# Optimization experiments

Hardware: AMD Instinct MI355X
Metric: run time of the kernel (lower is better)

The kernel has to match this reference:

```python
import jax, jax.numpy as jnp
import numpy as np

D = 1024
NUM_HEADS = 16
HEAD_DIM = D // NUM_HEADS
INIT_VALUES = 1e-4


def setup_inputs() -> dict:
    key = jax.random.key(0)
    ks = jax.random.split(key, 24)
    s = 0.02
    inp = {
        "v": jax.random.normal(ks[0], (8, 2048, D), dtype=jnp.float32),
        "l": jax.random.normal(ks[1], (8, 512, D), dtype=jnp.float32),
        "ln_v_g": jnp.ones((D,), jnp.float32),
        "ln_v_b": jnp.zeros((D,), jnp.float32),
        "ln_l_g": jnp.ones((D,), jnp.float32),
        "ln_l_b": jnp.zeros((D,), jnp.float32),
        "gamma_v": jnp.full((D,), INIT_VALUES, jnp.float32),
        "gamma_l": jnp.full((D,), INIT_VALUES, jnp.float32),
    }
    names = ["Wq_v2l", "Wk_v2l", "Wv_v2l", "Wo_v2l", "Wq_l2v", "Wk_l2v", "Wv_l2v", "Wo_l2v"]
    for i, n in enumerate(names):
        inp[n] = jax.random.normal(ks[2 + i], (D, D), dtype=jnp.float32) * s
        inp[n.replace("W", "b")] = jnp.zeros((D,), jnp.float32)
    return inp


def layer_norm(x, g, b, eps=1e-5):
    mu = jnp.mean(x, axis=-1, keepdims=True)
    var = jnp.var(x, axis=-1, keepdims=True)
    return (x - mu) * jax.lax.rsqrt(var + eps) * g + b


def mha(q_in, k_in, v_in, Wq, bq, Wk, bk, Wv, bv, Wo, bo):
    B, Sq, _ = q_in.shape
    Sk = k_in.shape[1]
    # torch Linear: x @ W.T + b
    q = (q_in @ Wq.T + bq).reshape(B, Sq, NUM_HEADS, HEAD_DIM)
    k = (k_in @ Wk.T + bk).reshape(B, Sk, NUM_HEADS, HEAD_DIM)
    v = (v_in @ Wv.T + bv).reshape(B, Sk, NUM_HEADS, HEAD_DIM)
    scores = jnp.einsum("bqhd,bkhd->bhqk", q, k) / np.sqrt(HEAD_DIM).astype(np.float32)
    attn = jax.nn.softmax(scores, axis=-1)
    ctx = jnp.einsum("bhqk,bkhd->bqhd", attn, v).reshape(B, Sq, D)
    return ctx @ Wo.T + bo


def reference(v, l, ln_v_g, ln_v_b, ln_l_g, ln_l_b, gamma_v, gamma_l,
              Wq_v2l, bq_v2l, Wk_v2l, bk_v2l, Wv_v2l, bv_v2l, Wo_v2l, bo_v2l,
              Wq_l2v, bq_l2v, Wk_l2v, bk_l2v, Wv_l2v, bv_l2v, Wo_l2v, bo_l2v):
    # eval mode: dropout and drop_path are identity
    v_norm = layer_norm(v, ln_v_g, ln_v_b)
    l_norm = layer_norm(l, ln_l_g, ln_l_b)
    updated_v = mha(v_norm, l_norm, l_norm,
                    Wq_v2l, bq_v2l, Wk_v2l, bk_v2l, Wv_v2l, bv_v2l, Wo_v2l, bo_v2l)
    updated_l = mha(l_norm, v_norm, v_norm,
                    Wq_l2v, bq_l2v, Wk_l2v, bk_l2v, Wv_l2v, bv_l2v, Wo_l2v, bo_l2v)
    v_out = v + gamma_v * updated_v
    l_out = l + gamma_l * updated_l
    return (v_out, l_out)
```

## Files before the change

kernel.cpp:

```cpp
#include <hip/hip_runtime.h>
#include <hip/hip_bf16.h>
#include <stdint.h>

typedef __bf16 bf16x8 __attribute__((ext_vector_type(8)));
typedef float f32x4 __attribute__((ext_vector_type(4)));
typedef float f32x16 __attribute__((ext_vector_type(16)));
typedef uint32_t u32x4 __attribute__((ext_vector_type(4)));
typedef unsigned short u16;

typedef __attribute__((address_space(1))) void as1_void;
typedef __attribute__((address_space(3))) void as3_void;

#define BAR() __builtin_amdgcn_s_barrier()
#define VMCNT(n) asm volatile("s_waitcnt vmcnt(" #n ")" ::: "memory")
#define LGKM0() asm volatile("s_waitcnt lgkmcnt(0)" ::: "memory")

__device__ __forceinline__ u16 f2bf(float f) {
  uint32_t u = __float_as_uint(f);
  u += 0x7fffu + ((u >> 16) & 1u);
  return (u16)(u >> 16);
}

struct Seg {
  const u16* W;
  const float* bias;
  u16* outb;
  float* outf;
  const float* res;
  const float* gamma;
  int mode;
  int sk;
  float ascale;
};

__global__ __launch_bounds__(256) void cvt8_kernel(
    const float4* s0, const float4* s1, const float4* s2, const float4* s3,
    const float4* s4, const float4* s5, const float4* s6, const float4* s7,
    ushort4* d0, ushort4* d1, ushort4* d2, ushort4* d3,
    ushort4* d4, ushort4* d5, ushort4* d6, ushort4* d7) {
  const float4* s; ushort4* d;
  switch (blockIdx.y) {
    case 0: s = s0; d = d0; break;
    case 1: s = s1; d = d1; break;
    case 2: s = s2; d = d2; break;
    case 3: s = s3; d = d3; break;
    case 4: s = s4; d = d4; break;
    case 5: s = s5; d = d5; break;
    case 6: s = s6; d = d6; break;
    default: s = s7; d = d7; break;
  }
  int i = blockIdx.x * 256 + threadIdx.x;
  float4 v = s[i];
  ushort4 o;
  o.x = f2bf(v.x); o.y = f2bf(v.y); o.z = f2bf(v.z); o.w = f2bf(v.w);
  d[i] = o;
}

__global__ __launch_bounds__(256) void ln_kernel(const float* __restrict__ x,
                                                 const float* __restrict__ g,
                                                 const float* __restrict__ b,
                                                 u16* __restrict__ out) {
  int row = blockIdx.x;
  int t = threadIdx.x;
  const float4* xr = (const float4*)(x + (size_t)row * 1024);
  float4 v = xr[t];
  float s = v.x + v.y + v.z + v.w;
  float s2 = v.x * v.x + v.y * v.y + v.z * v.z + v.w * v.w;
#pragma unroll
  for (int off = 1; off < 64; off <<= 1) {
    s += __shfl_xor(s, off);
    s2 += __shfl_xor(s2, off);
  }
  __shared__ float red[8];
  int wv = t >> 6;
  if ((t & 63) == 0) { red[wv] = s; red[4 + wv] = s2; }
  __syncthreads();
  s = red[0] + red[1] + red[2] + red[3];
  s2 = red[4] + red[5] + red[6] + red[7];
  float mu = s * (1.0f / 1024.0f);
  float var = s2 * (1.0f / 1024.0f) - mu * mu;
  float rstd = rsqrtf(var + 1e-5f);
  const float4 gv = ((const float4*)g)[t];
  const float4 bv = ((const float4*)b)[t];
  ushort4 o;
  o.x = f2bf((v.x - mu) * rstd * gv.x + bv.x);
  o.y = f2bf((v.y - mu) * rstd * gv.y + bv.y);
  o.z = f2bf((v.z - mu) * rstd * gv.z + bv.z);
  o.w = f2bf((v.w - mu) * rstd * gv.w + bv.w);
  ((ushort4*)out)[(size_t)row * 256 + t] = o;
}

__global__ __launch_bounds__(256, 3) void gemm_v7(
    const u16* __restrict__ A, Seg s0, Seg s1, Seg s2,
    int mtiles, int ntiles) {
  const int K = 1024;
  int hwid = blockIdx.x;
  int xcd = hwid & 7, q = hwid >> 3;
  int mchunk = mtiles >> 3;
  int mt = xcd * mchunk + q / ntiles;
  int nt = q % ntiles;
  int m0 = mt * 128;
  int si = nt >> 3;
  Seg seg = (si == 0) ? s0 : (si == 1) ? s1 : s2;
  int nl0 = (nt & 7) * 128;

  int t = threadIdx.x, lane = t & 63, wv = t >> 6;
  int wr = wv >> 1, wc = wv & 1;
  int lr = lane & 15, lg = lane >> 4;

  __shared__ u16 SA[3][128 * 32];
  __shared__ u16 SB[3][128 * 32];

  int row0 = t >> 2, c0 = t & 3;
  int sco = (c0 ^ ((row0 >> 1) & 3)) * 8;
  const u16* gA0 = A + (size_t)(m0 + row0) * K + sco;
  const u16* gB0 = seg.W + (size_t)(nl0 + row0) * K + sco;

  auto STAGE = [&](int slot, int kt) {
    __builtin_amdgcn_global_load_lds((const as1_void*)(gA0 + kt * 32),
                                     (as3_void*)(&SA[slot][0] + t * 8), 16, 0, 0);
    __builtin_amdgcn_global_load_lds((const as1_void*)(gA0 + (size_t)64 * K + kt * 32),
                                     (as3_void*)(&SA[slot][0] + 2048 + t * 8), 16, 0, 0);
    __builtin_amdgcn_global_load_lds((const as1_void*)(gB0 + kt * 32),
                                     (as3_void*)(&SB[slot][0] + t * 8), 16, 0, 0);
    __builtin_amdgcn_global_load_lds((const as1_void*)(gB0 + (size_t)64 * K + kt * 32),
                                     (as3_void*)(&SB[slot][0] + 2048 + t * 8), 16, 0, 0);
  };

  f32x4 acc[4][4] = {};

  STAGE(0, 0); STAGE(1, 1); STAGE(2, 2);
  VMCNT(8);
  BAR();

  int slot = 0;
  const int NKT = K / 32;
#pragma unroll 1
  for (int kt = 0; kt < NKT; ++kt) {
    bf16x8 aX[4], bX[4];
#pragma unroll
    for (int m = 0; m < 4; ++m) {
      int row = wr * 64 + m * 16 + lr;
      aX[m] = *(const bf16x8*)(&SA[slot][0] + row * 32 + ((lg ^ ((row >> 1) & 3)) * 8));
    }
#pragma unroll
    for (int n = 0; n < 4; ++n) {
      int row = wc * 64 + n * 16 + lr;
      bX[n] = *(const bf16x8*)(&SB[slot][0] + row * 32 + ((lg ^ ((row >> 1) & 3)) * 8));
    }
    LGKM0();
    BAR();
    if (kt + 3 < NKT) STAGE(slot, kt + 3);
    __builtin_amdgcn_s_setprio(1);
#pragma unroll
    for (int m = 0; m < 4; ++m)
#pragma unroll
      for (int n = 0; n < 4; ++n)
        acc[m][n] = __builtin_amdgcn_mfma_f32_16x16x32_bf16(aX[m], bX[n], acc[m][n], 0, 0, 0);
    __builtin_amdgcn_s_setprio(0);
    if (kt + 3 < NKT) { VMCNT(8); }
    else if (kt + 3 == NKT) { VMCNT(4); }
    else if (kt + 2 == NKT) { VMCNT(0); }
    BAR();
    slot = (slot == 2) ? 0 : slot + 1;
  }

  int rowb = m0 + wr * 64 + (lane >> 4) * 4;
#pragma unroll
  for (int m = 0; m < 4; ++m) {
#pragma unroll
    for (int n = 0; n < 4; ++n) {
      int scol = nl0 + wc * 64 + n * 16 + lr;
      float bcol = seg.bias[scol];
      int row = rowb + m * 16;
      if (seg.mode == 2) {
        int bb = row >> seg.sk;
        int ss = row & ((1 << seg.sk) - 1);
        int h = scol >> 6, d = scol & 63;
        ushort4 o;
        o.x = f2bf(acc[m][n][0] + bcol);
        o.y = f2bf(acc[m][n][1] + bcol);
        o.z = f2bf(acc[m][n][2] + bcol);
        o.w = f2bf(acc[m][n][3] + bcol);
        *(ushort4*)(seg.outb + ((((size_t)bb * 16 + h) * 64 + d) << seg.sk) + ss) = o;
      } else if (seg.mode == 0) {
#pragma unroll
        for (int r = 0; r < 4; ++r)
          seg.outb[(size_t)(row + r) * 1024 + scol] = f2bf((acc[m][n][r] + bcol) * seg.ascale);
      } else {
#pragma unroll
        for (int r = 0; r < 4; ++r) {
          size_t idx = (size_t)(row + r) * 1024 + scol;
          seg.outf[idx] = seg.res[idx] + seg.gamma[scol] * (acc[m][n][r] + bcol);
        }
      }
    }
  }
}

__global__ __launch_bounds__(256, 4) void attn_kernel(
    const u16* __restrict__ Q, const u16* __restrict__ Kmat,
    const u16* __restrict__ Vt, u16* __restrict__ ctx,
    int Sq, int Sk, int nq_shift) {
  int f = blockIdx.x;
  int xcd = f & 7, slot = f >> 3;
  int group = xcd * 16 + (slot >> nq_shift);
  int qt = slot & ((1 << nq_shift) - 1);
  int b = group >> 4, h = group & 15;
  int t = threadIdx.x, lane = t & 63, wv = t >> 6;
  int l31 = lane & 31, hi = lane >> 5;

  __shared__ u16 Ks[2][64 * 64];
  __shared__ u16 Vs[2][64 * 64];

  int q0 = qt * 128 + wv * 32;
  const u16* Qb = Q + (size_t)(b * Sq + q0 + l31) * 1024 + h * 64 + hi * 8;
  bf16x8 qf[4];
#pragma unroll
  for (int ds = 0; ds < 4; ++ds) qf[ds] = *(const bf16x8*)(Qb + ds * 16);

  int trow = t >> 3, tc = t & 7;
  int sc = (tc ^ (trow & 7)) * 8;
  const u16* gk = Kmat + (size_t)(b * Sk + trow) * 1024 + h * 64 + sc;
  const u16* gv = Vt + (size_t)((b * 16 + h) * 64 + trow) * Sk + sc;

  auto STAGE = [&](int buf, int kt) {
    const u16* k0 = gk + (size_t)(kt * 64) * 1024;
    const u16* v0 = gv + kt * 64;
    __builtin_amdgcn_global_load_lds((const as1_void*)k0, (as3_void*)(Ks[buf] + t * 8), 16, 0, 0);
    __builtin_amdgcn_global_load_lds((const as1_void*)(k0 + (size_t)32 * 1024), (as3_void*)(Ks[buf] + 2048 + t * 8), 16, 0, 0);
    __builtin_amdgcn_global_load_lds((const as1_void*)v0, (as3_void*)(Vs[buf] + t * 8), 16, 0, 0);
    __builtin_amdgcn_global_load_lds((const as1_void*)(v0 + (size_t)32 * Sk), (as3_void*)(Vs[buf] + 2048 + t * 8), 16, 0, 0);
  };

  STAGE(0, 0);
  __syncthreads();

  f32x16 acc0 = {}, acc1 = {};
  float m_run = -1e30f, l_run = 0.f;
  int sw = l31 & 7;

  int nt = Sk >> 6;
  for (int kt = 0; kt < nt; ++kt) {
    int cur = kt & 1;
    if (kt + 1 < nt) STAGE(cur ^ 1, kt + 1);
    const u16* kb = Ks[cur];
    f32x16 s0v = {}, s1v = {};
    __builtin_amdgcn_s_setprio(1);
#pragma unroll
    for (int ds = 0; ds < 4; ++ds) {
      int blk = 2 * ds + hi;
      bf16x8 ka0 = *(const bf16x8*)(kb + l31 * 64 + ((blk ^ sw) * 8));
      bf16x8 ka1 = *(const bf16x8*)(kb + (32 + l31) * 64 + ((blk ^ sw) * 8));
      s0v = __builtin_amdgcn_mfma_f32_32x32x16_bf16(ka0, qf[ds], s0v, 0, 0, 0);
      s1v = __builtin_amdgcn_mfma_f32_32x32x16_bf16(ka1, qf[ds], s1v, 0, 0, 0);
    }
    __builtin_amdgcn_s_setprio(0);
    float mx = s0v[0];
#pragma unroll
    for (int i = 1; i < 16; ++i) mx = fmaxf(mx, s0v[i]);
#pragma unroll
    for (int i = 0; i < 16; ++i) mx = fmaxf(mx, s1v[i]);
    mx = fmaxf(mx, __shfl_xor(mx, 32));
    if (__any(mx > m_run + 8.f)) {
      float mnew = fmaxf(m_run, mx);
      float fac = __builtin_amdgcn_exp2f(m_run - mnew);
#pragma unroll
      for (int r = 0; r < 16; ++r) {
        int src = (r & 3) + 8 * (r >> 2) + 4 * hi;
        float fr = __shfl(fac, src);
        acc0[r] *= fr;
        acc1[r] *= fr;
      }
      l_run *= fac;
      m_run = mnew;
    }
    float sum = 0.f;
#pragma unroll
    for (int i = 0; i < 16; ++i) {
      s0v[i] = __builtin_amdgcn_exp2f(s0v[i] - m_run);
      sum += s0v[i];
    }
#pragma unroll
    for (int i = 0; i < 16; ++i) {
      s1v[i] = __builtin_amdgcn_exp2f(s1v[i] - m_run);
      sum += s1v[i];
    }
    sum += __shfl_xor(sum, 32);
    l_run += sum;
    bf16x8 pa[4];
#pragma unroll
    for (int g = 0; g < 2; ++g) {
      const f32x16& s = g ? s1v : s0v;
#pragma unroll
      for (int half = 0; half < 2; ++half) {
        int o = half * 8;
        uint32_t a0, a1, b0, b1;
        asm("v_cvt_pk_bf16_f32 %0, %1, %2" : "=v"(a0) : "v"(s[o + 0]), "v"(s[o + 1]));
        asm("v_cvt_pk_bf16_f32 %0, %1, %2" : "=v"(a1) : "v"(s[o + 2]), "v"(s[o + 3]));
        asm("v_cvt_pk_bf16_f32 %0, %1, %2" : "=v"(b0) : "v"(s[o + 4]), "v"(s[o + 5]));
        asm("v_cvt_pk_bf16_f32 %0, %1, %2" : "=v"(b1) : "v"(s[o + 6]), "v"(s[o + 7]));
        asm("v_permlane32_swap_b32 %0, %1" : "+v"(a0), "+v"(b0));
        asm("v_permlane32_swap_b32 %0, %1" : "+v"(a1), "+v"(b1));
        u32x4 w;
        w[0] = a0; w[1] = a1; w[2] = b0; w[3] = b1;
        pa[g * 2 + half] = __builtin_bit_cast(bf16x8, w);
      }
    }
    const u16* vb = Vs[cur];
    __builtin_amdgcn_s_setprio(1);
#pragma unroll
    for (int ks = 0; ks < 4; ++ks) {
      int blk = 2 * ks + hi;
      bf16x8 vf0 = *(const bf16x8*)(vb + l31 * 64 + ((blk ^ sw) * 8));
      bf16x8 vf1 = *(const bf16x8*)(vb + (32 + l31) * 64 + ((blk ^ sw) * 8));
      acc0 = __builtin_amdgcn_mfma_f32_32x32x16_bf16(pa[ks], vf0, acc0, 0, 0, 0);
      acc1 = __builtin_amdgcn_mfma_f32_32x32x16_bf16(pa[ks], vf1, acc1, 0, 0, 0);
    }
    __builtin_amdgcn_s_setprio(0);
    __syncthreads();
  }
  float linv = 1.0f / l_run;
  u16* cb = ctx + (size_t)(b * Sq + q0) * 1024 + h * 64;
#pragma unroll
  for (int r = 0; r < 16; ++r) {
    int src = (r & 3) + 8 * (r >> 2) + 4 * hi;
    float li = __shfl(linv, src);
    cb[(size_t)src * 1024 + l31] = f2bf(acc0[r] * li);
    cb[(size_t)src * 1024 + 32 + l31] = f2bf(acc1[r] * li);
  }
}

extern "C" void kernel_launch(void* const* d_in, const int* in_sizes, int n_in,
                              void* d_out, int out_size, void* d_ws, size_t ws_size,
                              hipStream_t stream) {
  const float* v = (const float*)d_in[0];
  const float* l = (const float*)d_in[1];
  const float* ln_v_g = (const float*)d_in[2];
  const float* ln_v_b = (const float*)d_in[3];
  const float* ln_l_g = (const float*)d_in[4];
  const float* ln_l_b = (const float*)d_in[5];
  const float* gamma_v = (const float*)d_in[6];
  const float* gamma_l = (const float*)d_in[7];
  const float* Wf[8];
  const float* Bf[8];
  for (int i = 0; i < 8; ++i) {
    Wf[i] = (const float*)d_in[8 + 2 * i];
    Bf[i] = (const float*)d_in[9 + 2 * i];
  }
  float* v_out = (float*)d_out;
  float* l_out = v_out + (size_t)16384 * 1024;

  char* p = (char*)d_ws;
  auto alloc = [&](size_t bytes) {
    char* r = p;
    p += (bytes + 255) & ~(size_t)255;
    return r;
  };
  u16* Wbf[8];
  for (int i = 0; i < 8; ++i) Wbf[i] = (u16*)alloc((size_t)1024 * 1024 * 2);
  u16* vn   = (u16*)alloc((size_t)16384 * 1024 * 2);
  u16* lnm  = (u16*)alloc((size_t)4096 * 1024 * 2);
  u16* bufA = (u16*)alloc((size_t)16384 * 1024 * 2);
  u16* bufB = (u16*)alloc((size_t)4096 * 1024 * 2);
  u16* bufC = (u16*)alloc((size_t)4096 * 1024 * 2);
  u16* bufD = (u16*)alloc((size_t)16384 * 1024 * 2);
  u16* bufF = (u16*)alloc((size_t)4096 * 1024 * 2);
  u16* bufG = (u16*)alloc((size_t)16384 * 1024 * 2);

  const float QSC = 0.125f * 1.4426950408889634f;
  Seg zs = {};

  cvt8_kernel<<<dim3(1024, 8), 256, 0, stream>>>(
      (const float4*)Wf[0], (const float4*)Wf[1], (const float4*)Wf[2], (const float4*)Wf[3],
      (const float4*)Wf[4], (const float4*)Wf[5], (const float4*)Wf[6], (const float4*)Wf[7],
      (ushort4*)Wbf[0], (ushort4*)Wbf[1], (ushort4*)Wbf[2], (ushort4*)Wbf[3],
      (ushort4*)Wbf[4], (ushort4*)Wbf[5], (ushort4*)Wbf[6], (ushort4*)Wbf[7]);
  ln_kernel<<<16384, 256, 0, stream>>>(v, ln_v_g, ln_v_b, vn);
  ln_kernel<<<4096, 256, 0, stream>>>(l, ln_l_g, ln_l_b, lnm);

  {
    Seg a = {Wbf[4], Bf[4], bufB, nullptr, nullptr, nullptr, 0, 0, QSC};
    Seg b = {Wbf[1], Bf[1], bufF, nullptr, nullptr, nullptr, 0, 0, 1.0f};
    Seg c = {Wbf[2], Bf[2], bufC, nullptr, nullptr, nullptr, 2, 9, 1.0f};
    gemm_v7<<<dim3(768), 256, 0, stream>>>(lnm, a, b, c, 32, 24);
  }
  {
    Seg q = {Wbf[0], Bf[0], bufA, nullptr, nullptr, nullptr, 0, 0, QSC};
    Seg k = {Wbf[5], Bf[5], bufG, nullptr, nullptr, nullptr, 0, 0, 1.0f};
    Seg vv = {Wbf[6], Bf[6], bufD, nullptr, nullptr, nullptr, 2, 11, 1.0f};
    gemm_v7<<<dim3(3072), 256, 0, stream>>>(vn, q, k, vv, 128, 24);
  }
  attn_kernel<<<dim3(2048), 256, 0, stream>>>(bufA, bufF, bufC, bufA, 2048, 512, 4);
  {
    Seg o = {Wbf[3], Bf[3], nullptr, v_out, v, gamma_v, 1, 0, 1.0f};
    gemm_v7<<<dim3(1024), 256, 0, stream>>>(bufA, o, zs, zs, 128, 8);
  }
  attn_kernel<<<dim3(512), 256, 0, stream>>>(bufB, bufG, bufD, bufB, 512, 2048, 2);
  {
    Seg o = {Wbf[7], Bf[7], nullptr, l_out, l, gamma_l, 1, 0, 1.0f};
    gemm_v7<<<dim3(256), 256, 0, stream>>>(bufB, o, zs, zs, 32, 8);
  }
}
```

Baseline: 479.6 us.

## Merge paired GEMM and attention launches into grouped kernels; reorder pipeline waits

The two QKV projection GEMMs, the two attention passes, and the two output-projection GEMMs are each merged into a single launch, with block ids split between the two problems. This removes launch gaps and tail underutilisation, especially for the small language-side launches that cannot fill the GPU alone. The GEMM main loop also moves its LDS wait, barrier and next-stage prefetch to after the MFMA block, so only one barrier runs per iteration. The tighter vmcnt accounting changes how many loads are in flight before each barrier, which risks hazards or less overlap.

```diff
diff --git a/kernel.cpp b/kernel.cpp
--- a/kernel.cpp
+++ b/kernel.cpp
@@ -90,18 +90,27 @@
   ((ushort4*)out)[(size_t)row * 256 + t] = o;
 }
 
-__global__ __launch_bounds__(256, 3) void gemm_v7(
-    const u16* __restrict__ A, Seg s0, Seg s1, Seg s2,
-    int mtiles, int ntiles) {
+__global__ __launch_bounds__(256, 3) void gemm_v8(
+    const u16* __restrict__ A0, Seg s00, Seg s01, Seg s02, int mt0c, int nt0c,
+    const u16* __restrict__ A1, Seg s10, Seg s11, Seg s12, int mt1c, int nt1c) {
   const int K = 1024;
-  int hwid = blockIdx.x;
-  int xcd = hwid & 7, q = hwid >> 3;
+  int bid = blockIdx.x;
+  int nb0 = mt0c * nt0c;
+  const u16* A;
+  Seg sa, sb, sc;
+  int mtiles, ntiles, lbid;
+  if (bid < nb0) {
+    A = A0; mtiles = mt0c; ntiles = nt0c; lbid = bid; sa = s00; sb = s01; sc = s02;
+  } else {
+    A = A1; mtiles = mt1c; ntiles = nt1c; lbid = bid - nb0; sa = s10; sb = s11; sc = s12;
+  }
+  int xcd = lbid & 7, q = lbid >> 3;
   int mchunk = mtiles >> 3;
   int mt = xcd * mchunk + q / ntiles;
   int nt = q % ntiles;
   int m0 = mt * 128;
   int si = nt >> 3;
-  Seg seg = (si == 0) ? s0 : (si == 1) ? s1 : s2;
+  Seg seg = (si == 0) ? sa : (si == 1) ? sb : sc;
   int nl0 = (nt & 7) * 128;
 
   int t = threadIdx.x, lane = t & 63, wv = t >> 6;
@@ -148,9 +157,6 @@
       int row = wc * 64 + n * 16 + lr;
       bX[n] = *(const bf16x8*)(&SB[slot][0] + row * 32 + ((lg ^ ((row >> 1) & 3)) * 8));
     }
-    LGKM0();
-    BAR();
-    if (kt + 3 < NKT) STAGE(slot, kt + 3);
     __builtin_amdgcn_s_setprio(1);
 #pragma unroll
     for (int m = 0; m < 4; ++m)
@@ -158,10 +164,11 @@
       for (int n = 0; n < 4; ++n)
         acc[m][n] = __builtin_amdgcn_mfma_f32_16x16x32_bf16(aX[m], bX[n], acc[m][n], 0, 0, 0);
     __builtin_amdgcn_s_setprio(0);
-    if (kt + 3 < NKT) { VMCNT(8); }
-    else if (kt + 3 == NKT) { VMCNT(4); }
-    else if (kt + 2 == NKT) { VMCNT(0); }
+    LGKM0();
+    if (kt + 2 < NKT) { VMCNT(4); }
+    else if (kt + 1 < NKT) { VMCNT(0); }
     BAR();
+    if (kt + 3 < NKT) STAGE(slot, kt + 3);
     slot = (slot == 2) ? 0 : slot + 1;
   }
 
@@ -198,11 +205,20 @@
   }
 }
 
-__global__ __launch_bounds__(256, 4) void attn_kernel(
-    const u16* __restrict__ Q, const u16* __restrict__ Kmat,
-    const u16* __restrict__ Vt, u16* __restrict__ ctx,
-    int Sq, int Sk, int nq_shift) {
-  int f = blockIdx.x;
+__global__ __launch_bounds__(256, 4) void attn2_kernel(
+    const u16* __restrict__ Q0, const u16* __restrict__ K0,
+    const u16* __restrict__ V0, u16* __restrict__ C0, int Sq0, int Sk0, int nqs0, int nb0,
+    const u16* __restrict__ Q1, const u16* __restrict__ K1,
+    const u16* __restrict__ V1, u16* __restrict__ C1, int Sq1, int Sk1, int nqs1) {
+  int bid = blockIdx.x;
+  const u16 *Q, *Kmat, *Vt;
+  u16* ctx;
+  int Sq, Sk, nq_shift, f;
+  if (bid < nb0) {
+    Q = Q0; Kmat = K0; Vt = V0; ctx = C0; Sq = Sq0; Sk = Sk0; nq_shift = nqs0; f = bid;
+  } else {
+    Q = Q1; Kmat = K1; Vt = V1; ctx = C1; Sq = Sq1; Sk = Sk1; nq_shift = nqs1; f = bid - nb0;
+  }
   int xcd = f & 7, slot = f >> 3;
   int group = xcd * 16 + (slot >> nq_shift);
   int qt = slot & ((1 << nq_shift) - 1);
@@ -383,22 +399,19 @@
     Seg a = {Wbf[4], Bf[4], bufB, nullptr, nullptr, nullptr, 0, 0, QSC};
     Seg b = {Wbf[1], Bf[1], bufF, nullptr, nullptr, nullptr, 0, 0, 1.0f};
     Seg c = {Wbf[2], Bf[2], bufC, nullptr, nullptr, nullptr, 2, 9, 1.0f};
-    gemm_v7<<<dim3(768), 256, 0, stream>>>(lnm, a, b, c, 32, 24);
-  }
-  {
     Seg q = {Wbf[0], Bf[0], bufA, nullptr, nullptr, nullptr, 0, 0, QSC};
     Seg k = {Wbf[5], Bf[5], bufG, nullptr, nullptr, nullptr, 0, 0, 1.0f};
     Seg vv = {Wbf[6], Bf[6], bufD, nullptr, nullptr, nullptr, 2, 11, 1.0f};
-    gemm_v7<<<dim3(3072), 256, 0, stream>>>(vn, q, k, vv, 128, 24);
-  }
-  attn_kernel<<<dim3(2048), 256, 0, stream>>>(bufA, bufF, bufC, bufA, 2048, 512, 4);
+    gemm_v8<<<dim3(768 + 3072), 256, 0, stream>>>(lnm, a, b, c, 32, 24,
+                                                  vn, q, k, vv, 128, 24);
+  }
+  attn2_kernel<<<dim3(2048 + 512), 256, 0, stream>>>(
+      bufA, bufF, bufC, bufA, 2048, 512, 4, 2048,
+      bufB, bufG, bufD, bufB, 512, 2048, 2);
   {
-    Seg o = {Wbf[3], Bf[3], nullptr, v_out, v, gamma_v, 1, 0, 1.0f};
-    gemm_v7<<<dim3(1024), 256, 0, stream>>>(bufA, o, zs, zs, 128, 8);
-  }
-  attn_kernel<<<dim3(512), 256, 0, stream>>>(bufB, bufG, bufD, bufB, 512, 2048, 2);
-  {
-    Seg o = {Wbf[7], Bf[7], nullptr, l_out, l, gamma_l, 1, 0, 1.0f};
-    gemm_v7<<<dim3(256), 256, 0, stream>>>(bufB, o, zs, zs, 32, 8);
-  }
-}
+    Seg ov = {Wbf[3], Bf[3], nullptr, v_out, v, gamma_v, 1, 0, 1.0f};
+    Seg ol = {Wbf[7], Bf[7], nullptr, l_out, l, gamma_l, 1, 0, 1.0f};
+    gemm_v8<<<dim3(1024 + 256), 256, 0, stream>>>(bufA, ov, zs, zs, 128, 8,
+                                                  bufB, ol, zs, zs, 32, 8);
+  }
+}
```

Result: faster. 423.0 us (-11.8%).
